# Kernel tuning notes

Measured on AMD Instinct MI355X. Metric: run time of the kernel, lower is better.

Reference implementation:

```python
import jax, jax.numpy as jnp
import numpy as np

SPATIAL_SCALE = 0.125  # stride-8 FPN level
POINTS = 5


def _sample_points(bb):
    # bb: [N,H,W,5] = (cx, cy, w, h, theta) in image coords
    cx, cy, w, h, t = [bb[..., i] for i in range(5)]
    if POINTS == 1:
        px = cx[..., None]
        py = cy[..., None]
    else:
        vx = w * jnp.cos(t) * 0.5
        vy = w * jnp.sin(t) * 0.5
        wx = -h * jnp.sin(t) * 0.5
        wy = h * jnp.cos(t) * 0.5
        px = jnp.stack([cx, cx + vx + wx, cx - vx + wx, cx - vx - wx, cx + vx - wx], axis=-1)
        py = jnp.stack([cy, cy + vy + wy, cy - vy + wy, cy - vy - wy, cy + vy - wy], axis=-1)
    return px * SPATIAL_SCALE, py * SPATIAL_SCALE  # [N,H,W,P] feature-map coords


def _bilinear_gather(feat, y, x):
    # feat: [N,C,H,W]; y,x: [N,H,W,P] -> [N,H,W,P,C], mmcv-style bilinear w/ border rules
    N, C, H, W = feat.shape
    valid = (y >= -1.0) & (y <= H) & (x >= -1.0) & (x <= W)
    y = jnp.maximum(y, 0.0)
    x = jnp.maximum(x, 0.0)
    y_low = jnp.minimum(jnp.floor(y).astype(jnp.int32), H - 1)
    x_low = jnp.minimum(jnp.floor(x).astype(jnp.int32), W - 1)
    # if low index hits last row/col, snap coordinate onto it (ly/lx = 0)
    y = jnp.where(y_low >= H - 1, y_low.astype(feat.dtype), y)
    x = jnp.where(x_low >= W - 1, x_low.astype(feat.dtype), x)
    y_high = jnp.minimum(y_low + 1, H - 1)
    x_high = jnp.minimum(x_low + 1, W - 1)
    ly = y - y_low.astype(feat.dtype)
    lx = x - x_low.astype(feat.dtype)
    hy = 1.0 - ly
    hx = 1.0 - lx
    nn = jnp.arange(N)[:, None, None, None]  # broadcasts against [N,H,W,P]

    def g(yy, xx):
        return feat[nn, :, yy, xx]  # [N,H,W,P,C]

    val = ((hy * hx)[..., None] * g(y_low, x_low)
           + (hy * lx)[..., None] * g(y_low, x_high)
           + (ly * hx)[..., None] * g(y_high, x_low)
           + (ly * lx)[..., None] * g(y_high, x_high))
    return jnp.where(valid[..., None], val, 0.0)


def feature_refine(features, best_rbboxes):
    px, py = _sample_points(best_rbboxes)
    sampled = _bilinear_gather(features, py, px)       # [N,H,W,P,C]
    acc = sampled.sum(axis=3)                           # [N,H,W,C]
    return features + jnp.transpose(acc, (0, 3, 1, 2))  # [N,C,H,W]


def setup_inputs() -> dict:
    key = jax.random.key(0)
    k1, k2, k3, k4, k5, k6 = jax.random.split(key, 6)
    N, C, H, W = 4, 256, 128, 128
    IMG = 1024.0
    features = jax.random.normal(k1, (N, C, H, W), dtype=jnp.float32)
    cx = jax.random.uniform(k2, (N, H, W), minval=0.0, maxval=IMG)
    cy = jax.random.uniform(k3, (N, H, W), minval=0.0, maxval=IMG)
    bw = jax.random.uniform(k4, (N, H, W), minval=8.0, maxval=128.0)
    bh = jax.random.uniform(k5, (N, H, W), minval=8.0, maxval=128.0)
    th = jax.random.uniform(k6, (N, H, W), minval=-np.pi / 2, maxval=np.pi / 2)
    best_rbboxes = jnp.stack([cx, cy, bw, bh, th], axis=-1)  # [N,H,W,5]
    return {"features": features, "best_rbboxes": best_rbboxes}


def reference(features, best_rbboxes):
    return feature_refine(features, best_rbboxes)
```

## Files before the change

kernel.cpp:

```cpp
#include <hip/hip_runtime.h>


#define N_ 4
#define C_ 256
#define H_ 128
#define W_ 128
#define HW_ (H_ * W_)
#define SCALE 0.125f

typedef unsigned int uint32;

__device__ __forceinline__ uint32 f2bf(float f) {
    uint32 u = __float_as_uint(f);
    u = (u + 0x7FFF + ((u >> 16) & 1)) >> 16;
    return u;
}
__device__ __forceinline__ float blo(uint32 u) { return __uint_as_float(u << 16); }
__device__ __forceinline__ float bhi(uint32 u) { return __uint_as_float(u & 0xFFFF0000u); }

__global__ __launch_bounds__(1024) void nchw2nhwc_geo(const float* __restrict__ in,
                                                      const float* __restrict__ bb,
                                                      uint32* __restrict__ outU,
                                                      uint32* __restrict__ geoG)
{
    __shared__ uint32 tile[128 * 260];
    const int t   = threadIdx.x;
    const int l   = t & 63;
    const int g   = t >> 6;
    const int hw0 = blockIdx.x * 256;
    const int n   = blockIdx.y;

    if (t < 256) {
        const int px = n * HW_ + hw0 + t;
        const float* b = bb + (size_t)px * 5;
        const float cx = b[0], cy = b[1], bw = b[2], bh = b[3], th = b[4];
        const float st = sinf(th), ct = cosf(th);
        const float vx = bw * ct * 0.5f, vy = bw * st * 0.5f;
        const float wx = -bh * st * 0.5f, wy = bh * ct * 0.5f;
        const float pxs[5] = {cx, cx + vx + wx, cx - vx + wx, cx - vx - wx, cx + vx - wx};
        const float pys[5] = {cy, cy + vy + wy, cy - vy + wy, cy - vy - wy, cy + vy - wy};
        uint32* gw = geoG + (size_t)px * 32;
#pragma unroll
        for (int p = 0; p < 5; ++p) {
            float x = pxs[p] * SCALE;
            float y = pys[p] * SCALE;
            const bool valid = (y >= -1.0f) && (y <= (float)H_) &&
                               (x >= -1.0f) && (x <= (float)W_);
            y = fmaxf(y, 0.0f);
            x = fmaxf(x, 0.0f);
            int yl = min((int)y, H_ - 1);
            int xl = min((int)x, W_ - 1);
            if (yl >= H_ - 1) y = (float)yl;
            if (xl >= W_ - 1) x = (float)xl;
            const int yh = min(yl + 1, H_ - 1);
            const float ly = y - (float)yl, lx = x - (float)xl;
            const float hy = 1.0f - ly,     hx = 1.0f - lx;
            const int xa = min(xl, W_ - 2);
            float wA, wB;
            if (xl < W_ - 1) { wA = hx; wB = lx; }
            else             { wA = 0.0f; wB = 1.0f; }
            const float v = valid ? 1.0f : 0.0f;
            gw[p]      = (uint32)(yl * W_ + xa);
            gw[5 + p]  = (uint32)(yh * W_ + xa);
            gw[10 + p] = __float_as_uint(v * hy * wA);
            gw[15 + p] = __float_as_uint(v * hy * wB);
            gw[20 + p] = __float_as_uint(v * ly * wA);
            gw[25 + p] = __float_as_uint(v * ly * wB);
        }
        gw[30] = 0u; gw[31] = 0u;
    }

    const float* base = in + (size_t)n * C_ * HW_ + hw0 + 4 * l;
#pragma unroll
    for (int half = 0; half < 2; ++half) {
        float4 v0[4], v1[4];
#pragma unroll
        for (int r = 0; r < 4; ++r) {
            const int cp = g * 8 + half * 4 + r;
            v0[r] = *(const float4*)(base + (size_t)(2 * cp) * HW_);
            v1[r] = *(const float4*)(base + (size_t)(2 * cp + 1) * HW_);
        }
#pragma unroll
        for (int r = 0; r < 4; ++r) {
            const int cp = g * 8 + half * 4 + r;
            uint4 u;
            u.x = f2bf(v0[r].x) | (f2bf(v1[r].x) << 16);
            u.y = f2bf(v0[r].y) | (f2bf(v1[r].y) << 16);
            u.z = f2bf(v0[r].z) | (f2bf(v1[r].z) << 16);
            u.w = f2bf(v0[r].w) | (f2bf(v1[r].w) << 16);
            *(uint4*)&tile[cp * 260 + 4 * l] = u;
        }
    }
    __syncthreads();
    uint32* dst = outU + ((size_t)n * HW_ + hw0) * 128;
#pragma unroll 8
    for (int it = 0; it < 32; ++it) {
        const int f   = it * 1024 + t;
        const int row = f >> 7;
        const int q   = f & 127;
        dst[f] = tile[q * 260 + row];
    }
}

__global__ __launch_bounds__(256, 4) void fr_refine(const uint32* __restrict__ nhwcU,
                                                    const uint32* __restrict__ geoG,
                                                    float* __restrict__ out)
{
    __shared__ float tile[32 * 260];
    const int t  = threadIdx.x;
    const int l  = t & 63;
    const int wv = __builtin_amdgcn_readfirstlane(t >> 6);
    const int bx = blockIdx.x;
    const int xcd = bx & 7;
    const int n   = xcd >> 1;
    const int s   = bx >> 3;
    const int h   = ((xcd & 1) << 6) | (s >> 2);
    const int w0  = (s & 3) * 32;

    const float idsel = (l < 32) ? 1.0f : 0.0f;
    const uint32* plane = nhwcU + (size_t)n * HW_ * 128;
    const int hwb = h * W_ + w0 + wv * 8;
    const uint32* gb = geoG + ((size_t)n * HW_ + hwb) * 32;
    const int vl4 = 4 * l;

    for (int p = 0; p < 8; ++p) {
        const uint32* g = gb + p * 32;
        const int hwp = hwb + p;

        int o0[5], o1[5];
#pragma unroll
        for (int q = 0; q < 5; ++q) { o0[q] = (int)g[q]; o1[q] = (int)g[5 + q]; }

        const uint4 rid = *(const uint4*)(plane + (size_t)hwp * 128 + vl4);
        uint4 r0[5], r1[5];
#pragma unroll
        for (int q = 0; q < 5; ++q) {
            r0[q] = *(const uint4*)(plane + (size_t)o0[q] * 128 + vl4);
            r1[q] = *(const uint4*)(plane + (size_t)o1[q] * 128 + vl4);
        }

        float a[8];
        a[0] = idsel * blo(rid.x); a[1] = idsel * bhi(rid.x);
        a[2] = idsel * blo(rid.y); a[3] = idsel * bhi(rid.y);
        a[4] = idsel * blo(rid.z); a[5] = idsel * bhi(rid.z);
        a[6] = idsel * blo(rid.w); a[7] = idsel * bhi(rid.w);

#pragma unroll
        for (int q = 0; q < 5; ++q) {
            const float w00 = __uint_as_float(g[10 + q]);
            const float w01 = __uint_as_float(g[15 + q]);
            const float w10 = __uint_as_float(g[20 + q]);
            const float w11 = __uint_as_float(g[25 + q]);
            const float wr0 = (l < 32) ? w00 : w01;
            const float wr1 = (l < 32) ? w10 : w11;
            a[0] = fmaf(wr0, blo(r0[q].x), a[0]); a[1] = fmaf(wr0, bhi(r0[q].x), a[1]);
            a[2] = fmaf(wr0, blo(r0[q].y), a[2]); a[3] = fmaf(wr0, bhi(r0[q].y), a[3]);
            a[4] = fmaf(wr0, blo(r0[q].z), a[4]); a[5] = fmaf(wr0, bhi(r0[q].z), a[5]);
            a[6] = fmaf(wr0, blo(r0[q].w), a[6]); a[7] = fmaf(wr0, bhi(r0[q].w), a[7]);
            a[0] = fmaf(wr1, blo(r1[q].x), a[0]); a[1] = fmaf(wr1, bhi(r1[q].x), a[1]);
            a[2] = fmaf(wr1, blo(r1[q].y), a[2]); a[3] = fmaf(wr1, bhi(r1[q].y), a[3]);
            a[4] = fmaf(wr1, blo(r1[q].z), a[4]); a[5] = fmaf(wr1, bhi(r1[q].z), a[5]);
            a[6] = fmaf(wr1, blo(r1[q].w), a[6]); a[7] = fmaf(wr1, bhi(r1[q].w), a[7]);
        }
#pragma unroll
        for (int k = 0; k < 8; ++k) a[k] += __shfl_xor(a[k], 32, 64);
        if (l < 32) {
            const int pxl = wv * 8 + p;
            float* dst = &tile[pxl * 260 + 8 * l];
            *(float4*)dst       = make_float4(a[0], a[1], a[2], a[3]);
            *(float4*)(dst + 4) = make_float4(a[4], a[5], a[6], a[7]);
        }
    }
    __syncthreads();
    const size_t obase = (size_t)n * C_ * HW_ + h * W_ + w0;
#pragma unroll 4
    for (int it = 0; it < 32; ++it) {
        const int flat = it * 256 + t;
        const int px = flat & 31;
        const int c  = flat >> 5;
        out[obase + (size_t)c * HW_ + px] = tile[px * 260 + c];
    }
}

__global__ __launch_bounds__(256) void fr_kernel(
    const float* __restrict__ feat,
    const float* __restrict__ bb,
    float* __restrict__ out)
{
    const int lane = threadIdx.x & 63;
    const int wave = threadIdx.x >> 6;
    const int tile = blockIdx.x;
    const int wt   = tile & 1;
    const int h    = (tile >> 1) & (H_ - 1);
    const int n    = tile >> 8;
    const int w    = wt * 64 + lane;
    const int cb   = blockIdx.y;

    const float* b = bb + (size_t)((n * H_ + h) * W_ + w) * 5;
    const float cx = b[0], cy = b[1], bw = b[2], bh = b[3], th = b[4];
    const float st = sinf(th), ct = cosf(th);
    const float vx = bw * ct * 0.5f, vy = bw * st * 0.5f;
    const float wx = -bh * st * 0.5f, wy = bh * ct * 0.5f;
    const float pxs[5] = {cx, cx + vx + wx, cx - vx + wx, cx - vx - wx, cx + vx - wx};
    const float pys[5] = {cy, cy + vy + wy, cy - vy + wy, cy - vy - wy, cy + vy - wy};

    int   off0[5], off1[5];
    float wgt[20];
#pragma unroll
    for (int p = 0; p < 5; ++p) {
        float x = pxs[p] * SCALE;
        float y = pys[p] * SCALE;
        const bool valid = (y >= -1.0f) && (y <= (float)H_) &&
                           (x >= -1.0f) && (x <= (float)W_);
        y = fmaxf(y, 0.0f);
        x = fmaxf(x, 0.0f);
        int yl = min((int)y, H_ - 1);
        int xl = min((int)x, W_ - 1);
        if (yl >= H_ - 1) y = (float)yl;
        if (xl >= W_ - 1) x = (float)xl;
        const int yh = min(yl + 1, H_ - 1);
        const float ly = y - (float)yl, lx = x - (float)xl;
        const float hy = 1.0f - ly,     hx = 1.0f - lx;
        const int xa = min(xl, W_ - 2);
        float wA, wB;
        if (xl < W_ - 1) { wA = hx; wB = lx; }
        else             { wA = 0.0f; wB = 1.0f; }
        const float v = valid ? 1.0f : 0.0f;
        off0[p] = yl * W_ + xa;
        off1[p] = yh * W_ + xa;
        wgt[p * 4 + 0] = v * hy * wA;
        wgt[p * 4 + 1] = v * hy * wB;
        wgt[p * 4 + 2] = v * ly * wA;
        wgt[p * 4 + 3] = v * ly * wB;
    }

    const int hw = h * W_ + w;
    const size_t planeBase = ((size_t)n * C_ + cb * 64 + wave * 16) * HW_;
    const float* fp = feat + planeBase;
    float*       op = out  + planeBase;
    for (int it = 0; it < 16; ++it) {
        float acc = fp[hw];
#pragma unroll
        for (int p = 0; p < 5; ++p) {
            acc += wgt[p * 4 + 0] * fp[off0[p]]
                 + wgt[p * 4 + 1] * fp[off0[p] + 1]
                 + wgt[p * 4 + 2] * fp[off1[p]]
                 + wgt[p * 4 + 3] * fp[off1[p] + 1];
        }
        op[hw] = acc;
        fp += HW_;
        op += HW_;
    }
}

extern "C" void kernel_launch(void* const* d_in, const int* in_sizes, int n_in,
                              void* d_out, int out_size, void* d_ws, size_t ws_size,
                              hipStream_t stream) {
    const float* feat = (const float*)d_in[0];
    const float* bbox = (const float*)d_in[1];
    float* out = (float*)d_out;

    const size_t nhwcBytes = (size_t)N_ * HW_ * C_ * 2;
    const size_t geoBytes  = (size_t)N_ * HW_ * 32 * 4;
    if (ws_size >= nhwcBytes + geoBytes) {
        uint32* nhwcU = (uint32*)d_ws;
        uint32* geoG  = (uint32*)((char*)d_ws + nhwcBytes);
        nchw2nhwc_geo<<<dim3(HW_ / 256, N_), dim3(1024), 0, stream>>>(feat, bbox, nhwcU, geoG);
        fr_refine<<<dim3(N_ * H_ * (W_ / 32)), dim3(256), 0, stream>>>(nhwcU, geoG, out);
    } else {
        dim3 grid(N_ * H_ * (W_ / 64), C_ / 64, 1);
        fr_kernel<<<grid, dim3(256), 0, stream>>>(feat, bbox, out);
    }
}
```

Baseline: 175.4 us.

## Split channels into two halves across blocks in both transpose and refine kernels

Both the NCHW-to-NHWC bf16 transpose and the gather/refine kernel now handle 128 channels per block instead of 256, which doubles the grid and halves shared memory per block. In the refine kernel each lane now loads 8 bytes instead of 16 per tap, the per-tap weights are hoisted, and an XOR swizzle replaces padding in the output tile. The aim is higher occupancy and more blocks in flight to hide gather latency. In exchange, the geometry and index loads are repeated for each channel half and each gather request is narrower.

```diff
diff --git a/kernel.cpp b/kernel.cpp
--- a/kernel.cpp
+++ b/kernel.cpp
@@ -18,19 +18,20 @@
 __device__ __forceinline__ float blo(uint32 u) { return __uint_as_float(u << 16); }
 __device__ __forceinline__ float bhi(uint32 u) { return __uint_as_float(u & 0xFFFF0000u); }
 
-__global__ __launch_bounds__(1024) void nchw2nhwc_geo(const float* __restrict__ in,
-                                                      const float* __restrict__ bb,
-                                                      uint32* __restrict__ outU,
-                                                      uint32* __restrict__ geoG)
+__global__ __launch_bounds__(1024, 8) void nchw2nhwc_geo(const float* __restrict__ in,
+                                                         const float* __restrict__ bb,
+                                                         uint32* __restrict__ outU,
+                                                         uint32* __restrict__ geoG)
 {
-    __shared__ uint32 tile[128 * 260];
+    __shared__ uint32 tile[64 * 260];
     const int t   = threadIdx.x;
     const int l   = t & 63;
     const int g   = t >> 6;
     const int hw0 = blockIdx.x * 256;
-    const int n   = blockIdx.y;
-
-    if (t < 256) {
+    const int ch  = blockIdx.y;
+    const int n   = blockIdx.z;
+
+    if (ch == 0 && t < 256) {
         const int px = n * HW_ + hw0 + t;
         const float* b = bb + (size_t)px * 5;
         const float cx = b[0], cy = b[1], bw = b[2], bh = b[3], th = b[4];
@@ -70,115 +71,112 @@
         gw[30] = 0u; gw[31] = 0u;
     }
 
-    const float* base = in + (size_t)n * C_ * HW_ + hw0 + 4 * l;
-#pragma unroll
-    for (int half = 0; half < 2; ++half) {
-        float4 v0[4], v1[4];
-#pragma unroll
-        for (int r = 0; r < 4; ++r) {
-            const int cp = g * 8 + half * 4 + r;
-            v0[r] = *(const float4*)(base + (size_t)(2 * cp) * HW_);
-            v1[r] = *(const float4*)(base + (size_t)(2 * cp + 1) * HW_);
-        }
-#pragma unroll
-        for (int r = 0; r < 4; ++r) {
-            const int cp = g * 8 + half * 4 + r;
-            uint4 u;
-            u.x = f2bf(v0[r].x) | (f2bf(v1[r].x) << 16);
-            u.y = f2bf(v0[r].y) | (f2bf(v1[r].y) << 16);
-            u.z = f2bf(v0[r].z) | (f2bf(v1[r].z) << 16);
-            u.w = f2bf(v0[r].w) | (f2bf(v1[r].w) << 16);
-            *(uint4*)&tile[cp * 260 + 4 * l] = u;
-        }
+    const float* base = in + (size_t)n * C_ * HW_ + (size_t)(ch * 128) * HW_ + hw0 + 4 * l;
+    float4 v0[4], v1[4];
+#pragma unroll
+    for (int r = 0; r < 4; ++r) {
+        const int cp = g * 4 + r;
+        v0[r] = *(const float4*)(base + (size_t)(2 * cp) * HW_);
+        v1[r] = *(const float4*)(base + (size_t)(2 * cp + 1) * HW_);
+    }
+#pragma unroll
+    for (int r = 0; r < 4; ++r) {
+        const int cp = g * 4 + r;
+        uint4 u;
+        u.x = f2bf(v0[r].x) | (f2bf(v1[r].x) << 16);
+        u.y = f2bf(v0[r].y) | (f2bf(v1[r].y) << 16);
+        u.z = f2bf(v0[r].z) | (f2bf(v1[r].z) << 16);
+        u.w = f2bf(v0[r].w) | (f2bf(v1[r].w) << 16);
+        *(uint4*)&tile[cp * 260 + 4 * l] = u;
     }
     __syncthreads();
-    uint32* dst = outU + ((size_t)n * HW_ + hw0) * 128;
-#pragma unroll 8
-    for (int it = 0; it < 32; ++it) {
+    uint32* dst = outU + ((size_t)n * HW_ + hw0) * 128 + ch * 64;
+#pragma unroll
+    for (int it = 0; it < 16; ++it) {
         const int f   = it * 1024 + t;
-        const int row = f >> 7;
-        const int q   = f & 127;
-        dst[f] = tile[q * 260 + row];
-    }
-}
-
-__global__ __launch_bounds__(256, 4) void fr_refine(const uint32* __restrict__ nhwcU,
+        const int row = f >> 6;
+        const int q   = f & 63;
+        dst[(size_t)row * 128 + q] = tile[q * 260 + row];
+    }
+}
+
+__global__ __launch_bounds__(256, 8) void fr_refine(const uint32* __restrict__ nhwcU,
                                                     const uint32* __restrict__ geoG,
                                                     float* __restrict__ out)
 {
-    __shared__ float tile[32 * 260];
+    __shared__ float tile[32 * 128];
     const int t  = threadIdx.x;
     const int l  = t & 63;
     const int wv = __builtin_amdgcn_readfirstlane(t >> 6);
     const int bx = blockIdx.x;
     const int xcd = bx & 7;
     const int n   = xcd >> 1;
+    const int ch  = xcd & 1;
     const int s   = bx >> 3;
-    const int h   = ((xcd & 1) << 6) | (s >> 2);
+    const int h   = s >> 2;
     const int w0  = (s & 3) * 32;
 
-    const float idsel = (l < 32) ? 1.0f : 0.0f;
+    const int lh = l >> 5;
+    const int lw = l & 31;
+    const int lofs = (lh << 7) + (ch << 6) + (lw << 1);
+    const float idsel = lh ? 0.0f : 1.0f;
     const uint32* plane = nhwcU + (size_t)n * HW_ * 128;
     const int hwb = h * W_ + w0 + wv * 8;
     const uint32* gb = geoG + ((size_t)n * HW_ + hwb) * 32;
-    const int vl4 = 4 * l;
-
+
+#pragma unroll 1
     for (int p = 0; p < 8; ++p) {
         const uint32* g = gb + p * 32;
-        const int hwp = hwb + p;
 
         int o0[5], o1[5];
-#pragma unroll
-        for (int q = 0; q < 5; ++q) { o0[q] = (int)g[q]; o1[q] = (int)g[5 + q]; }
-
-        const uint4 rid = *(const uint4*)(plane + (size_t)hwp * 128 + vl4);
-        uint4 r0[5], r1[5];
+        float wr0[5], wr1[5];
 #pragma unroll
         for (int q = 0; q < 5; ++q) {
-            r0[q] = *(const uint4*)(plane + (size_t)o0[q] * 128 + vl4);
-            r1[q] = *(const uint4*)(plane + (size_t)o1[q] * 128 + vl4);
-        }
-
-        float a[8];
+            o0[q] = (int)g[q];
+            o1[q] = (int)g[5 + q];
+            wr0[q] = lh ? __uint_as_float(g[15 + q]) : __uint_as_float(g[10 + q]);
+            wr1[q] = lh ? __uint_as_float(g[25 + q]) : __uint_as_float(g[20 + q]);
+        }
+
+        const uint2 rid = *(const uint2*)(plane + (size_t)(hwb + p) * 128 + lofs);
+        uint2 r0[5], r1[5];
+#pragma unroll
+        for (int q = 0; q < 5; ++q) {
+            r0[q] = *(const uint2*)(plane + (size_t)o0[q] * 128 + lofs);
+            r1[q] = *(const uint2*)(plane + (size_t)o1[q] * 128 + lofs);
+        }
+        __builtin_amdgcn_sched_barrier(0);
+
+        float a[4];
         a[0] = idsel * blo(rid.x); a[1] = idsel * bhi(rid.x);
         a[2] = idsel * blo(rid.y); a[3] = idsel * bhi(rid.y);
-        a[4] = idsel * blo(rid.z); a[5] = idsel * bhi(rid.z);
-        a[6] = idsel * blo(rid.w); a[7] = idsel * bhi(rid.w);
-
 #pragma unroll
         for (int q = 0; q < 5; ++q) {
-            const float w00 = __uint_as_float(g[10 + q]);
-            const float w01 = __uint_as_float(g[15 + q]);
-            const float w10 = __uint_as_float(g[20 + q]);
-            const float w11 = __uint_as_float(g[25 + q]);
-            const float wr0 = (l < 32) ? w00 : w01;
-            const float wr1 = (l < 32) ? w10 : w11;
-            a[0] = fmaf(wr0, blo(r0[q].x), a[0]); a[1] = fmaf(wr0, bhi(r0[q].x), a[1]);
-            a[2] = fmaf(wr0, blo(r0[q].y), a[2]); a[3] = fmaf(wr0, bhi(r0[q].y), a[3]);
-            a[4] = fmaf(wr0, blo(r0[q].z), a[4]); a[5] = fmaf(wr0, bhi(r0[q].z), a[5]);
-            a[6] = fmaf(wr0, blo(r0[q].w), a[6]); a[7] = fmaf(wr0, bhi(r0[q].w), a[7]);
-            a[0] = fmaf(wr1, blo(r1[q].x), a[0]); a[1] = fmaf(wr1, bhi(r1[q].x), a[1]);
-            a[2] = fmaf(wr1, blo(r1[q].y), a[2]); a[3] = fmaf(wr1, bhi(r1[q].y), a[3]);
-            a[4] = fmaf(wr1, blo(r1[q].z), a[4]); a[5] = fmaf(wr1, bhi(r1[q].z), a[5]);
-            a[6] = fmaf(wr1, blo(r1[q].w), a[6]); a[7] = fmaf(wr1, bhi(r1[q].w), a[7]);
-        }
-#pragma unroll
-        for (int k = 0; k < 8; ++k) a[k] += __shfl_xor(a[k], 32, 64);
+            a[0] = fmaf(wr0[q], blo(r0[q].x), a[0]);
+            a[1] = fmaf(wr0[q], bhi(r0[q].x), a[1]);
+            a[2] = fmaf(wr0[q], blo(r0[q].y), a[2]);
+            a[3] = fmaf(wr0[q], bhi(r0[q].y), a[3]);
+            a[0] = fmaf(wr1[q], blo(r1[q].x), a[0]);
+            a[1] = fmaf(wr1[q], bhi(r1[q].x), a[1]);
+            a[2] = fmaf(wr1[q], blo(r1[q].y), a[2]);
+            a[3] = fmaf(wr1[q], bhi(r1[q].y), a[3]);
+        }
+#pragma unroll
+        for (int k = 0; k < 4; ++k) a[k] += __shfl_xor(a[k], 32, 64);
         if (l < 32) {
-            const int pxl = wv * 8 + p;
-            float* dst = &tile[pxl * 260 + 8 * l];
-            *(float4*)dst       = make_float4(a[0], a[1], a[2], a[3]);
-            *(float4*)(dst + 4) = make_float4(a[4], a[5], a[6], a[7]);
+            const int px = wv * 8 + p;
+            const int c0 = (lw * 4) ^ ((px & 7) << 2);
+            *(float4*)&tile[px * 128 + c0] = make_float4(a[0], a[1], a[2], a[3]);
         }
     }
     __syncthreads();
-    const size_t obase = (size_t)n * C_ * HW_ + h * W_ + w0;
-#pragma unroll 4
-    for (int it = 0; it < 32; ++it) {
+    const size_t obase = (size_t)n * C_ * HW_ + (size_t)(ch * 128) * HW_ + h * W_ + w0;
+#pragma unroll
+    for (int it = 0; it < 16; ++it) {
         const int flat = it * 256 + t;
         const int px = flat & 31;
         const int c  = flat >> 5;
-        out[obase + (size_t)c * HW_ + px] = tile[px * 260 + c];
+        out[obase + (size_t)c * HW_ + px] = tile[px * 128 + (c ^ ((px & 7) << 2))];
     }
 }
 
@@ -265,8 +263,8 @@
     if (ws_size >= nhwcBytes + geoBytes) {
         uint32* nhwcU = (uint32*)d_ws;
         uint32* geoG  = (uint32*)((char*)d_ws + nhwcBytes);
-        nchw2nhwc_geo<<<dim3(HW_ / 256, N_), dim3(1024), 0, stream>>>(feat, bbox, nhwcU, geoG);
-        fr_refine<<<dim3(N_ * H_ * (W_ / 32)), dim3(256), 0, stream>>>(nhwcU, geoG, out);
+        nchw2nhwc_geo<<<dim3(HW_ / 256, 2, N_), dim3(1024), 0, stream>>>(feat, bbox, nhwcU, geoG);
+        fr_refine<<<dim3(N_ * H_ * (W_ / 32) * 2), dim3(256), 0, stream>>>(nhwcU, geoG, out);
     } else {
         dim3 grid(N_ * H_ * (W_ / 64), C_ / 64, 1);
         fr_kernel<<<grid, dim3(256), 0, stream>>>(feat, bbox, out);
```

After: 181.0 us. +3.2%, slower.
